# Optimization experiments

Hardware: AMD Instinct MI355X
Metric: run time of the kernel (lower is better)

Reference implementation:

```python
import jax, jax.numpy as jnp
import numpy as np

B, S, T, D = 64, 256, 8, 256
E, M = 500000, 2048
NEG_INF = -10000000000.0


def setup_inputs() -> dict:
    key = jax.random.key(0)
    ks = jax.random.split(key, 9)
    token_reprs = jax.random.normal(ks[0], (B, S, T, D), dtype=jnp.float32)
    w1 = jax.random.normal(ks[1], (D, D // 2), dtype=jnp.float32) * (1.0 / np.sqrt(D))
    b1 = jnp.zeros((D // 2,), dtype=jnp.float32)
    w2 = jax.random.normal(ks[2], (D // 2, 1), dtype=jnp.float32) * (1.0 / np.sqrt(D // 2))
    b2 = jnp.zeros((1,), dtype=jnp.float32)
    edge_index = jax.random.randint(ks[3], (2, E), 0, B * S, dtype=jnp.int32)
    lm_indices = jax.random.randint(ks[4], (M,), 0, B * S * T, dtype=jnp.int32)
    batch_pointers = jax.random.randint(ks[5], (M,), 0, B, dtype=jnp.int32)
    tree_padding_mask = jax.random.randint(ks[6], (B, S), 0, 2, dtype=jnp.int32).astype(jnp.bool_)
    return {
        "token_reprs": token_reprs,
        "w1": w1, "b1": b1, "w2": w2, "b2": b2,
        "edge_index": edge_index,
        "lm_indices": lm_indices,
        "batch_pointers": batch_pointers,
        "tree_padding_mask": tree_padding_mask,
    }


def reference(token_reprs, w1, b1, w2, b2, edge_index, lm_indices, batch_pointers, tree_padding_mask):
    b, s, t, d = token_reprs.shape
    # type representation is the first token of each type tree
    type_reprs = token_reprs[:, :, 0]                  # [B, S, D]
    flat_types = type_reprs.reshape(b * s, d)          # [B*S, D]

    # predict_lemmas: gather scope/goal reprs, elementwise multiply, 2-layer MLP
    scope_ids, goal_ids = edge_index[0], edge_index[1]
    h = flat_types[scope_ids] * flat_types[goal_ids]   # [E, D]
    h = h @ w1 + b1                                    # [E, D//2] (Dropout is identity in eval)
    lemmas = (h @ w2 + b2)[:, 0]                       # [E]

    # predict_masks: gather masked token reprs + per-tree candidates, dot, mask
    mask_reprs = token_reprs.reshape(b * s * t, d)[lm_indices]  # [M, D]
    candidates = type_reprs[batch_pointers]            # [M, S, D]
    candidate_mask = tree_padding_mask[batch_pointers] # [M, S]
    lm_preds = jnp.einsum('md,msd->ms', mask_reprs, candidates)
    lm_preds = jnp.where(candidate_mask, lm_preds, NEG_INF)
    return lemmas, lm_preds
```

## Files before the change

kernel.cpp:

```cpp
#include <hip/hip_runtime.h>

#define DD 256
#define SS 256
#define BB 64
#define NEDGE 500000
#define MM 2048
#define NEG_INF -10000000000.0f
#define ROWF4 512
#define NROWS (BB * SS)

#define EPB0 256
#define NCHUNK ((NEDGE + EPB0 - 1) / EPB0)
#define NBLK_E (8 * (NCHUNK / 2))
#define PPAD 500224

#define OFF_VC     0
#define OFF_MSORT  4096
#define OFF_BSTART (4096 + MM * 4)
#define OFF_ASLAB  (1 << 16)
#define OFF_P2     ((1 << 16) + (8 << 20))
#define OFF_MROWS  ((1 << 16) + (16 << 20))
#define OFF_PART   ((1 << 16) + (17 << 20))

typedef float vf4 __attribute__((ext_vector_type(4)));

__device__ __forceinline__ float bflo(unsigned u) { return __uint_as_float(u << 16); }
__device__ __forceinline__ float bfhi(unsigned u) { return __uint_as_float(u & 0xFFFF0000u); }
__device__ __forceinline__ unsigned short bf_rne(float f) {
    unsigned u = __float_as_uint(f);
    return (unsigned short)((u + 0x7FFFu + ((u >> 16) & 1u)) >> 16);
}
__device__ __forceinline__ unsigned pack2_rne(float a, float b) {
    return (unsigned)bf_rne(a) | ((unsigned)bf_rne(b) << 16);
}

__global__ void setup_k(const float* __restrict__ w1, const float* __restrict__ b1,
                        const float* __restrict__ w2, const float* __restrict__ b2,
                        const int* __restrict__ bp,
                        float* __restrict__ vc, int* __restrict__ msorted,
                        int* __restrict__ bstart) {
    const int t = threadIdx.x;
    if (blockIdx.x == 0) {
        __shared__ float sw2[DD / 2];
        if (t < DD / 2) sw2[t] = w2[t];
        __syncthreads();
        const int lane = t & 63, w = t >> 6;
        for (int r = w; r < DD; r += 4) {
            float x = w1[r * (DD / 2) + lane] * sw2[lane]
                    + w1[r * (DD / 2) + 64 + lane] * sw2[64 + lane];
            x += __shfl_down(x, 32);
            x += __shfl_down(x, 16);
            x += __shfl_down(x, 8);
            x += __shfl_down(x, 4);
            x += __shfl_down(x, 2);
            x += __shfl_down(x, 1);
            if (lane == 0) vc[r] = x;
        }
        if (w == 0) {
            float x = b1[lane] * sw2[lane] + b1[64 + lane] * sw2[64 + lane];
            x += __shfl_down(x, 32);
            x += __shfl_down(x, 16);
            x += __shfl_down(x, 8);
            x += __shfl_down(x, 4);
            x += __shfl_down(x, 2);
            x += __shfl_down(x, 1);
            if (lane == 0) vc[DD] = x + b2[0];
        }
    } else {
        __shared__ int hist[BB];
        __shared__ int offs[BB + 1];
        if (t < BB) hist[t] = 0;
        __syncthreads();
        for (int m = t; m < MM; m += 256) atomicAdd(&hist[bp[m]], 1);
        __syncthreads();
        if (t == 0) {
            int acc = 0;
            for (int i = 0; i < BB; ++i) { offs[i] = acc; acc += hist[i]; }
            offs[BB] = acc;
        }
        __syncthreads();
        if (t < BB + 1) bstart[t] = offs[t];
        __syncthreads();
        for (int m = t; m < MM; m += 256) {
            int pos = atomicAdd(&offs[bp[m]], 1);
            msorted[pos] = m;
        }
    }
}

__global__ __launch_bounds__(256) void compact(
        const float* __restrict__ tok, const int* __restrict__ lmi,
        unsigned* __restrict__ aslab,
        unsigned* __restrict__ p2, unsigned* __restrict__ mrows) {
    const int lane = threadIdx.x & 63;
    const int w    = threadIdx.x >> 6;
    if (blockIdx.x < NROWS / 4) {
        const int row = blockIdx.x * 4 + w;
        const float4 a = ((const float4*)tok)[(size_t)row * ROWF4 + lane];
        unsigned p0 = pack2_rne(a.x, a.y), p1 = pack2_rne(a.z, a.w);
        const int k = lane >> 3, sub = lane & 7;
        const size_t si = (size_t)(k * NROWS + row) * 16 + sub * 2;
        aslab[si] = p0; aslab[si + 1] = p1;
        const size_t pi = (size_t)row * 128 + lane * 2;
        p2[pi] = p0; p2[pi + 1] = p1;
    } else {
        const int m = (blockIdx.x - NROWS / 4) * 4 + w;
        const float4 a = ((const float4*)(tok + (size_t)lmi[m] * DD))[lane];
        mrows[(size_t)m * 128 + lane * 2]     = pack2_rne(a.x, a.y);
        mrows[(size_t)m * 128 + lane * 2 + 1] = pack2_rne(a.z, a.w);
    }
}

__global__ __launch_bounds__(256) void edge_part(
        const unsigned* __restrict__ aslab,
        const int* __restrict__ edges, const float* __restrict__ vc,
        float* __restrict__ pp) {
    const int b = blockIdx.x;
    const int xcd = b & 7;
    const int p = xcd >> 1;
    const int chunk = (b >> 3) * 2 + (xcd & 1);
    const int e0 = chunk * EPB0;
    const int k0 = p * 2;

    const int t = threadIdx.x;
    const int lane = t & 63, w = t >> 6;
    const int sub = lane & 7, j = lane >> 3;
    __shared__ int sIdx[2][EPB0];
    __shared__ float accs[EPB0];
    const int e = e0 + t;
    const bool val = e < NEDGE;
    sIdx[0][t] = val ? __builtin_nontemporal_load(edges + e) : 0;
    sIdx[1][t] = val ? __builtin_nontemporal_load(edges + NEDGE + e) : 0;

    const float4 v0 = ((const float4*)vc)[k0 * 8 + sub];
    const float4 v1 = ((const float4*)vc)[(k0 + 1) * 8 + sub];
    __syncthreads();

    float acc[8];
    #pragma unroll
    for (int i = 0; i < 8; ++i) acc[i] = 0.f;
    const int slotbase = w * 64 + j;

    int offS[8], offG[8];
    #pragma unroll
    for (int i = 0; i < 8; ++i) {
        const int slot = slotbase + i * 8;
        offS[i] = sIdx[0][slot] * 16;
        offG[i] = sIdx[1][slot] * 16;
    }

    #pragma unroll 1
    for (int kk = 0; kk < 2; ++kk) {
        const int k = k0 + kk;
        const unsigned* base = aslab + (size_t)k * (NROWS * 16) + sub * 2;
        const float4 v = kk ? v1 : v0;
        #pragma unroll
        for (int i = 0; i < 8; ++i) {
            const uint2 pu = *(const uint2*)(base + offS[i]);
            const uint2 qu = *(const uint2*)(base + offG[i]);
            acc[i] += (bflo(pu.x) * bflo(qu.x)) * v.x
                    + (bfhi(pu.x) * bfhi(qu.x)) * v.y
                    + (bflo(pu.y) * bflo(qu.y)) * v.z
                    + (bfhi(pu.y) * bfhi(qu.y)) * v.w;
        }
    }
    #pragma unroll
    for (int i = 0; i < 8; ++i) {
        float x = acc[i];
        x += __shfl_down(x, 4, 8);
        x += __shfl_down(x, 2, 8);
        x += __shfl_down(x, 1, 8);
        if (sub == 0) accs[slotbase + i * 8] = x;
    }
    __syncthreads();
    if (val) pp[(size_t)p * PPAD + e] = accs[t];
}

__global__ __launch_bounds__(256) void combine(
        const float* __restrict__ pp, const float* __restrict__ vc,
        float* __restrict__ out) {
    const int i = blockIdx.x * 256 + threadIdx.x;
    if (i >= NEDGE / 4) return;
    const float c = vc[DD];
    vf4 a = ((const vf4*)pp)[i];
    vf4 b = ((const vf4*)(pp + PPAD))[i];
    vf4 d = ((const vf4*)(pp + 2 * (size_t)PPAD))[i];
    vf4 e = ((const vf4*)(pp + 3 * (size_t)PPAD))[i];
    vf4 r = a + b + d + e + c;
    __builtin_nontemporal_store(r, (vf4*)out + i);
}

__global__ __launch_bounds__(256) void lm_gemm(
        const unsigned* __restrict__ p2,
        const unsigned* __restrict__ mrows,
        const int* __restrict__ msorted,
        const int* __restrict__ bstart,
        const int* __restrict__ tpm,
        float* __restrict__ out) {
    const int b  = blockIdx.x;
    const int st = blockIdx.y;
    const int ch = blockIdx.z;
    const int s0 = bstart[b], s1 = bstart[b + 1];
    const int base = s0 + ch * 32;
    if (base >= s1) return;
    const int nm = min(32, s1 - base);
    const int t = threadIdx.x;

    __shared__ unsigned lmaskU[32 * 132];
    __shared__ unsigned srowU[32 * 132];
    __shared__ int mids[32];
    __shared__ int sact[64];
    __shared__ int snact;

    if (t < 32) mids[t] = msorted[base + min(t, nm - 1)];
    if (t >= 64 && t < 128) {
        int lt = t - 64;
        bool act = tpm[b * SS + st * 64 + lt] != 0;
        unsigned long long mk = __ballot(act);
        if (act) sact[__popcll(mk & ((1ull << lt) - 1))] = lt;
        if (lt == 0) snact = (int)__popcll(mk);
    }
    __syncthreads();

    for (int f = t; f < nm * 32; f += 256) {
        int r = f >> 5, q = f & 31;
        *(uint4*)&lmaskU[r * 132 + q * 4] = ((const uint4*)mrows)[(size_t)mids[r] * 32 + q];
    }
    for (int f = t; f < nm * 64; f += 256) {
        int i = f >> 6, c = f & 63;
        if (!tpm[b * SS + st * 64 + c])
            out[(size_t)mids[i] * SS + st * 64 + c] = NEG_INF;
    }
    __syncthreads();

    const int nact = snact;
    const int i2 = t & 15, sg = t >> 4;

    for (int g = 0; g * 32 < nact; ++g) {
        if (g) __syncthreads();
        const int nv = min(32, nact - g * 32);
        for (int f = t; f < nv * 32; f += 256) {
            int r = f >> 5, q = f & 31;
            size_t row = (size_t)b * SS + st * 64 + sact[g * 32 + r];
            *(uint4*)&srowU[r * 132 + q * 4] = ((const uint4*)p2)[row * 32 + q];
        }
        __syncthreads();

        float a00 = 0.f, a01 = 0.f, a10 = 0.f, a11 = 0.f;
        #pragma unroll 4
        for (int stp = 0; stp < 32; ++stp) {
            const uint4 A0 = *(const uint4*)&lmaskU[i2 * 132 + stp * 4];
            const uint4 A1 = *(const uint4*)&lmaskU[(i2 + 16) * 132 + stp * 4];
            const uint4 B0 = *(const uint4*)&srowU[sg * 132 + stp * 4];
            const uint4 B1 = *(const uint4*)&srowU[(sg + 16) * 132 + stp * 4];
            float a0[8], a1[8], b0[8], b1[8];
            a0[0] = bflo(A0.x); a0[1] = bfhi(A0.x); a0[2] = bflo(A0.y); a0[3] = bfhi(A0.y);
            a0[4] = bflo(A0.z); a0[5] = bfhi(A0.z); a0[6] = bflo(A0.w); a0[7] = bfhi(A0.w);
            a1[0] = bflo(A1.x); a1[1] = bfhi(A1.x); a1[2] = bflo(A1.y); a1[3] = bfhi(A1.y);
            a1[4] = bflo(A1.z); a1[5] = bfhi(A1.z); a1[6] = bflo(A1.w); a1[7] = bfhi(A1.w);
            b0[0] = bflo(B0.x); b0[1] = bfhi(B0.x); b0[2] = bflo(B0.y); b0[3] = bfhi(B0.y);
            b0[4] = bflo(B0.z); b0[5] = bfhi(B0.z); b0[6] = bflo(B0.w); b0[7] = bfhi(B0.w);
            b1[0] = bflo(B1.x); b1[1] = bfhi(B1.x); b1[2] = bflo(B1.y); b1[3] = bfhi(B1.y);
            b1[4] = bflo(B1.z); b1[5] = bfhi(B1.z); b1[6] = bflo(B1.w); b1[7] = bfhi(B1.w);
            #pragma unroll
            for (int jj = 0; jj < 8; ++jj) {
                a00 = fmaf(a0[jj], b0[jj], a00);
                a01 = fmaf(a0[jj], b1[jj], a01);
                a10 = fmaf(a1[jj], b0[jj], a10);
                a11 = fmaf(a1[jj], b1[jj], a11);
            }
        }

        const int iA = g * 32 + sg, iB = iA + 16;
        if (i2 < nm) {
            size_t ob = (size_t)mids[i2] * SS + st * 64;
            if (iA < nact) out[ob + sact[iA]] = a00;
            if (iB < nact) out[ob + sact[iB]] = a01;
        }
        if (i2 + 16 < nm) {
            size_t ob = (size_t)mids[i2 + 16] * SS + st * 64;
            if (iA < nact) out[ob + sact[iA]] = a10;
            if (iB < nact) out[ob + sact[iB]] = a11;
        }
    }
}

extern "C" void kernel_launch(void* const* d_in, const int* in_sizes, int n_in,
                              void* d_out, int out_size, void* d_ws, size_t ws_size,
                              hipStream_t stream) {
    const float* tok = (const float*)d_in[0];
    const float* w1  = (const float*)d_in[1];
    const float* b1  = (const float*)d_in[2];
    const float* w2  = (const float*)d_in[3];
    const float* b2  = (const float*)d_in[4];
    const int* edges = (const int*)d_in[5];
    const int* lmi   = (const int*)d_in[6];
    const int* bp    = (const int*)d_in[7];
    const int* tpm   = (const int*)d_in[8];

    float* out_lemmas = (float*)d_out;
    float* out_lm     = (float*)d_out + NEDGE;

    char* ws = (char*)d_ws;
    float* vc        = (float*)(ws + OFF_VC);
    int* msorted     = (int*)(ws + OFF_MSORT);
    int* bstart      = (int*)(ws + OFF_BSTART);
    unsigned* aslab  = (unsigned*)(ws + OFF_ASLAB);
    unsigned* p2     = (unsigned*)(ws + OFF_P2);
    unsigned* mrows  = (unsigned*)(ws + OFF_MROWS);
    float* pp        = (float*)(ws + OFF_PART);

    setup_k<<<2, 256, 0, stream>>>(w1, b1, w2, b2, bp, vc, msorted, bstart);
    compact<<<NROWS / 4 + MM / 4, 256, 0, stream>>>(tok, lmi, aslab, p2, mrows);
    edge_part<<<NBLK_E, 256, 0, stream>>>(aslab, edges, vc, pp);
    combine<<<(NEDGE / 4 + 255) / 256, 256, 0, stream>>>(pp, vc, out_lemmas);
    lm_gemm<<<dim3(BB, 4, 8), 256, 0, stream>>>(p2, mrows, msorted, bstart, tpm, out_lm);
}
```

Measured before the change: 287.7 us.

## Claim edge chunks dynamically per XCD, drop duplicate p2 copy, nontemporal partial stores

```diff
diff --git a/kernel.cpp b/kernel.cpp
--- a/kernel.cpp
+++ b/kernel.cpp
@@ -11,14 +11,14 @@
 
 #define EPB0 256
 #define NCHUNK ((NEDGE + EPB0 - 1) / EPB0)
-#define NBLK_E (8 * (NCHUNK / 2))
+#define NBLK_E (4 * NCHUNK)
 #define PPAD 500224
 
 #define OFF_VC     0
+#define OFF_CNT    2048
 #define OFF_MSORT  4096
 #define OFF_BSTART (4096 + MM * 4)
 #define OFF_ASLAB  (1 << 16)
-#define OFF_P2     ((1 << 16) + (8 << 20))
 #define OFF_MROWS  ((1 << 16) + (16 << 20))
 #define OFF_PART   ((1 << 16) + (17 << 20))
 
@@ -38,7 +38,7 @@
                         const float* __restrict__ w2, const float* __restrict__ b2,
                         const int* __restrict__ bp,
                         float* __restrict__ vc, int* __restrict__ msorted,
-                        int* __restrict__ bstart) {
+                        int* __restrict__ bstart, int* __restrict__ cnt) {
     const int t = threadIdx.x;
     if (blockIdx.x == 0) {
         __shared__ float sw2[DD / 2];
@@ -69,6 +69,7 @@
     } else {
         __shared__ int hist[BB];
         __shared__ int offs[BB + 1];
+        if (t < 4) cnt[t] = 0;
         if (t < BB) hist[t] = 0;
         __syncthreads();
         for (int m = t; m < MM; m += 256) atomicAdd(&hist[bp[m]], 1);
@@ -90,8 +91,7 @@
 
 __global__ __launch_bounds__(256) void compact(
         const float* __restrict__ tok, const int* __restrict__ lmi,
-        unsigned* __restrict__ aslab,
-        unsigned* __restrict__ p2, unsigned* __restrict__ mrows) {
+        unsigned* __restrict__ aslab, unsigned* __restrict__ mrows) {
     const int lane = threadIdx.x & 63;
     const int w    = threadIdx.x >> 6;
     if (blockIdx.x < NROWS / 4) {
@@ -101,8 +101,6 @@
         const int k = lane >> 3, sub = lane & 7;
         const size_t si = (size_t)(k * NROWS + row) * 16 + sub * 2;
         aslab[si] = p0; aslab[si + 1] = p1;
-        const size_t pi = (size_t)row * 128 + lane * 2;
-        p2[pi] = p0; p2[pi + 1] = p1;
     } else {
         const int m = (blockIdx.x - NROWS / 4) * 4 + w;
         const float4 a = ((const float4*)(tok + (size_t)lmi[m] * DD))[lane];
@@ -114,15 +112,30 @@
 __global__ __launch_bounds__(256) void edge_part(
         const unsigned* __restrict__ aslab,
         const int* __restrict__ edges, const float* __restrict__ vc,
-        float* __restrict__ pp) {
-    const int b = blockIdx.x;
-    const int xcd = b & 7;
-    const int p = xcd >> 1;
-    const int chunk = (b >> 3) * 2 + (xcd & 1);
+        float* __restrict__ pp, int* __restrict__ cnt) {
+    __shared__ int sclaim;
+    const int t = threadIdx.x;
+    if (t == 0) {
+        unsigned xcc;
+        asm volatile("s_getreg_b32 %0, hwreg(HW_REG_XCC_ID)" : "=s"(xcc));
+        const int p0 = (int)(xcc >> 1) & 3;
+        int got = -1;
+        #pragma unroll 1
+        for (int jj = 0; jj < 4; ++jj) {
+            const int p = (p0 + jj) & 3;
+            const int pos = atomicAdd(&cnt[p], 1);
+            if (pos < NCHUNK) { got = p * NCHUNK + pos; break; }
+        }
+        sclaim = got;
+    }
+    __syncthreads();
+    const int claim = sclaim;
+    if (claim < 0) return;
+    const int p = claim / NCHUNK;
+    const int chunk = claim - p * NCHUNK;
     const int e0 = chunk * EPB0;
     const int k0 = p * 2;
 
-    const int t = threadIdx.x;
     const int lane = t & 63, w = t >> 6;
     const int sub = lane & 7, j = lane >> 3;
     __shared__ int sIdx[2][EPB0];
@@ -173,7 +186,7 @@
         if (sub == 0) accs[slotbase + i * 8] = x;
     }
     __syncthreads();
-    if (val) pp[(size_t)p * PPAD + e] = accs[t];
+    if (val) __builtin_nontemporal_store(accs[t], pp + (size_t)p * PPAD + e);
 }
 
 __global__ __launch_bounds__(256) void combine(
@@ -191,7 +204,7 @@
 }
 
 __global__ __launch_bounds__(256) void lm_gemm(
-        const unsigned* __restrict__ p2,
+        const unsigned* __restrict__ aslab,
         const unsigned* __restrict__ mrows,
         const int* __restrict__ msorted,
         const int* __restrict__ bstart,
@@ -242,7 +255,8 @@
         for (int f = t; f < nv * 32; f += 256) {
             int r = f >> 5, q = f & 31;
             size_t row = (size_t)b * SS + st * 64 + sact[g * 32 + r];
-            *(uint4*)&srowU[r * 132 + q * 4] = ((const uint4*)p2)[row * 32 + q];
+            *(uint4*)&srowU[r * 132 + q * 4] =
+                ((const uint4*)aslab)[((size_t)(q >> 2) * NROWS + row) * 4 + (q & 3)];
         }
         __syncthreads();
 
@@ -303,16 +317,16 @@
 
     char* ws = (char*)d_ws;
     float* vc        = (float*)(ws + OFF_VC);
+    int* cnt         = (int*)(ws + OFF_CNT);
     int* msorted     = (int*)(ws + OFF_MSORT);
     int* bstart      = (int*)(ws + OFF_BSTART);
     unsigned* aslab  = (unsigned*)(ws + OFF_ASLAB);
-    unsigned* p2     = (unsigned*)(ws + OFF_P2);
     unsigned* mrows  = (unsigned*)(ws + OFF_MROWS);
     float* pp        = (float*)(ws + OFF_PART);
 
-    setup_k<<<2, 256, 0, stream>>>(w1, b1, w2, b2, bp, vc, msorted, bstart);
-    compact<<<NROWS / 4 + MM / 4, 256, 0, stream>>>(tok, lmi, aslab, p2, mrows);
-    edge_part<<<NBLK_E, 256, 0, stream>>>(aslab, edges, vc, pp);
+    setup_k<<<2, 256, 0, stream>>>(w1, b1, w2, b2, bp, vc, msorted, bstart, cnt);
+    compact<<<NROWS / 4 + MM / 4, 256, 0, stream>>>(tok, lmi, aslab, mrows);
+    edge_part<<<NBLK_E, 256, 0, stream>>>(aslab, edges, vc, pp, cnt);
     combine<<<(NEDGE / 4 + 255) / 256, 256, 0, stream>>>(pp, vc, out_lemmas);
-    lm_gemm<<<dim3(BB, 4, 8), 256, 0, stream>>>(p2, mrows, msorted, bstart, tpm, out_lm);
-}
+    lm_gemm<<<dim3(BB, 4, 8), 256, 0, stream>>>(aslab, mrows, msorted, bstart, tpm, out_lm);
+}
```

Result: slower. 344.3 us (+19.7%).
